# Kernel tuning notes

Hardware: AMD Instinct MI355X
Metric: run time of the kernel (lower is better)

Reference implementation:

```python
import jax, jax.numpy as jnp
import numpy as np

KNN_K = 8
WINDOW = 3  # temporal_window + 1 candidate frames
LN_EPS = 1e-5
NORM_EPS = 1e-12


def setup_inputs() -> dict:
    key = jax.random.key(0)
    B, T, M, D, H = 2, 8, 512, 1024, 1024
    ks = jax.random.split(key, 12)
    s = 0.02
    return {
        "z": jax.random.normal(ks[0], (B, T, M, D), jnp.float32),
        "Wq": jax.random.normal(ks[1], (D, D), jnp.float32) * s,
        "Wv": jax.random.normal(ks[2], (D, D), jnp.float32) * s,
        "Wout": jax.random.normal(ks[3], (D, D), jnp.float32) * s,
        "ln_w": jnp.ones((D,), jnp.float32),
        "ln_b": jnp.zeros((D,), jnp.float32),
        "Watt_q": jax.random.normal(ks[4], (D, D), jnp.float32) * s,
        "Watt_k": jax.random.normal(ks[5], (D, D), jnp.float32) * s,
        "W_ih": jax.random.normal(ks[6], (3 * H, D), jnp.float32) * s,
        "W_hh": jax.random.normal(ks[7], (3 * H, H), jnp.float32) * s,
        "b_ih": jnp.zeros((3 * H,), jnp.float32),
        "b_hh": jnp.zeros((3 * H,), jnp.float32),
        "W_mf": jax.random.normal(ks[8], (D, H), jnp.float32) * s,
        "b_mf": jnp.zeros((D,), jnp.float32),
    }


def _forward(z, Wq, Wv, Wout, ln_w, ln_b, Watt_q, Watt_k,
             W_ih, W_hh, b_ih, b_hh, W_mf, b_mf):
    B, T, M, D = z.shape
    H = W_hh.shape[1]
    # cosine normalization (torch F.normalize with eps clamp)
    zn = z / jnp.maximum(jnp.linalg.norm(z, axis=-1, keepdims=True), NORM_EPS)
    mem = jnp.zeros((B, M, H), z.dtype)
    b_ar = jnp.arange(B)[:, None, None]
    outs = []
    for t in range(T):  # T is static; fully vectorized over B, M, k inside
        tts = t - jnp.arange(WINDOW)          # candidate frames t, t-1, t-2
        valid = tts >= 0                      # [W]
        cand = zn[:, jnp.clip(tts, 0)]        # [B,W,M,D]
        # cosine similarity query nodes at t vs all candidates (dt-major order)
        sim = jnp.einsum('bmd,bwnd->bmwn', zn[:, t], cand).reshape(B, M, WINDOW * M)
        sim = jnp.where(jnp.repeat(valid, M)[None, None, :], sim, -jnp.inf)
        vals, idx = jax.lax.top_k(sim, KNN_K)  # [B,M,k]
        dt = idx // M
        j = idx % M
        tt = jnp.clip(t - dt, 0)
        Kfeat = z[b_ar, tt, j]                 # [B,M,k,D] gathered neighbors
        # GAT quirk faithful to source: scalar logit scale from node 0's query,
        # first output coordinate only, shared across all nodes of (b,t)
        s0 = z[:, t, 0] @ Watt_q[0]            # [B]
        kh_sum = (Kfeat @ Watt_k.T).sum(-1)    # [B,M,k]
        att = jax.nn.softmax(s0[:, None, None] * kh_sum, axis=-1)
        alpha = 0.5 * vals + 0.5 * att         # [B,M,k]
        msg = jnp.einsum('bmk,bmkd->bmd', alpha, Kfeat @ Wv.T)
        h_t = z[:, t]                          # [B,M,D]
        x = msg + h_t @ Wq.T
        mu = x.mean(-1, keepdims=True)
        var = ((x - mu) ** 2).mean(-1, keepdims=True)
        x = (x - mu) / jnp.sqrt(var + LN_EPS) * ln_w + ln_b
        inp = x @ Wout.T
        # torch GRUCell: gates ordered (r, z, n)
        gi = inp @ W_ih.T + b_ih               # [B,M,3H]
        gh = mem @ W_hh.T + b_hh
        ir, iz, inn = jnp.split(gi, 3, axis=-1)
        hr, hz, hn = jnp.split(gh, 3, axis=-1)
        r = jax.nn.sigmoid(ir + hr)
        zg = jax.nn.sigmoid(iz + hz)
        n = jnp.tanh(inn + r * hn)
        mem = (1.0 - zg) * n + zg * mem
        outs.append(h_t + mem @ W_mf.T + b_mf)
    h = jnp.stack(outs, axis=1)                # [B,T,M,D]
    return h, mem


def reference(z, Wq, Wv, Wout, ln_w, ln_b, Watt_q, Watt_k,
              W_ih, W_hh, b_ih, b_hh, W_mf, b_mf):
    return _forward(z, Wq, Wv, Wout, ln_w, ln_b, Watt_q, Watt_k,
                    W_ih, W_hh, b_ih, b_hh, W_mf, b_mf)
```

## Files before the change

### kernel.cpp

```cpp
#include <hip/hip_runtime.h>
#include <hip/hip_bf16.h>
#include <math.h>

#define B_ 2
#define T_ 8
#define M_ 512
#define D_ 1024
#define H_ 1024
#define NC_ 1536
#define KNN 8

typedef __hip_bfloat16 bf16;
typedef short v8s __attribute__((ext_vector_type(8)));
typedef float v4f __attribute__((ext_vector_type(4)));

__device__ __forceinline__ float b2f(short s) {
  union { unsigned u; float f; } x; x.u = ((unsigned)(unsigned short)s) << 16; return x.f;
}
__device__ __forceinline__ short f2b(float f) {
  bf16 h = __float2bfloat16(f); return *(short*)&h;
}

__device__ __forceinline__ void async16(const void* g, void* l) {
  __builtin_amdgcn_global_load_lds(
      (const __attribute__((address_space(1))) void*)g,
      (__attribute__((address_space(3))) void*)l, 16, 0, 0);
}

__device__ __forceinline__ void mfma_loop(const bf16* __restrict__ A,
                                          const bf16* __restrict__ Bp,
                                          int K, v4f (&acc)[4][4],
                                          bf16* sA, bf16* sB)
{
  const int tid  = threadIdx.x;
  const int lane = tid & 63;
  const int wave = tid >> 6;
  const int quad = lane >> 4;
  const int l15  = lane & 15;
  const int wr = (wave >> 1) * 64;
  const int wc = (wave & 1) * 64;

  const int r0 = tid >> 2, g0 = (tid & 3) ^ ((r0 >> 1) & 3);
  const int c1 = tid + 256;
  const int r1 = c1 >> 2,  g1 = (c1 & 3) ^ ((r1 >> 1) & 3);

  const bf16* a0p = A  + (size_t)r0*K + g0*8;
  const bf16* a1p = A  + (size_t)r1*K + g1*8;
  const bf16* b0p = Bp + (size_t)r0*K + g0*8;
  const bf16* b1p = Bp + (size_t)r1*K + g1*8;
  bf16* la0 = sA + tid*8;  bf16* la1 = sA + c1*8;
  bf16* lb0 = sB + tid*8;  bf16* lb1 = sB + c1*8;

  int aoff[4], boff[4];
  #pragma unroll
  for (int i = 0; i < 4; ++i) {
    int ra = wr + i*16 + l15;
    aoff[i] = (ra*4 + (quad ^ ((ra >> 1) & 3))) * 8;
    int rb = wc + i*16 + l15;
    boff[i] = (rb*4 + (quad ^ ((rb >> 1) & 3))) * 8;
  }

  for (int k0 = 0; k0 < K; k0 += 32) {
    __syncthreads();
    async16(a0p + k0, la0);
    async16(a1p + k0, la1);
    async16(b0p + k0, lb0);
    async16(b1p + k0, lb1);
    __syncthreads();
    v8s af[4], bfr[4];
    #pragma unroll
    for (int i = 0; i < 4; ++i) af[i]  = *(const v8s*)(sA + aoff[i]);
    #pragma unroll
    for (int i = 0; i < 4; ++i) bfr[i] = *(const v8s*)(sB + boff[i]);
    #pragma unroll
    for (int mi = 0; mi < 4; ++mi)
      #pragma unroll
      for (int ni = 0; ni < 4; ++ni)
        acc[mi][ni] = __builtin_amdgcn_mfma_f32_16x16x32_bf16(
            af[mi], bfr[ni], acc[mi][ni], 0, 0, 0);
  }
}

__device__ __forceinline__ void out_tile(int oid, int tp,
    const bf16* __restrict__ memhb, const bf16* __restrict__ Wmfb,
    const float* __restrict__ b_mf, const float* __restrict__ z,
    float* __restrict__ out, bf16* sA, bf16* sB)
{
  const int rb = oid >> 3, cb = oid & 7;
  const int g0 = (rb >> 2)*4096 + tp*512 + (rb & 3)*128;
  v4f acc[4][4];
  #pragma unroll
  for (int i = 0; i < 4; ++i)
    #pragma unroll
    for (int j = 0; j < 4; ++j) acc[i][j] = (v4f){0.f,0.f,0.f,0.f};
  mfma_loop(memhb + (size_t)g0*H_, Wmfb + (size_t)(cb*128)*H_, H_, acc, sA, sB);
  const int tid = threadIdx.x, lane = tid & 63, wave = tid >> 6;
  const int quad = lane >> 4, l15 = lane & 15;
  const int wr = (wave >> 1) * 64, wcc = (wave & 1) * 64;
  #pragma unroll
  for (int ni = 0; ni < 4; ++ni) {
    const int col = cb*128 + wcc + ni*16 + l15;
    const float bv = b_mf[col];
    #pragma unroll
    for (int mi = 0; mi < 4; ++mi) {
      const int rowb = g0 + wr + mi*16 + quad*4;
      #pragma unroll
      for (int reg = 0; reg < 4; ++reg) {
        const int row = rowb + reg;
        out[(size_t)row*D_ + col] = acc[mi][ni][reg] + bv + z[(size_t)row*D_ + col];
      }
    }
  }
}

template<bool DUAL, bool STATS>
__global__ __launch_bounds__(256) void k_bgemm(
    const bf16* __restrict__ A1, const bf16* __restrict__ B1,
    const bf16* __restrict__ A2, const bf16* __restrict__ B2,
    bf16* __restrict__ Cv, int N, int K,
    float* __restrict__ ssum, float* __restrict__ ssq)
{
  __shared__ bf16 sA[128*32];
  __shared__ bf16 sB[128*32];
  v4f acc[4][4];
  #pragma unroll
  for (int i = 0; i < 4; ++i)
    #pragma unroll
    for (int j = 0; j < 4; ++j) acc[i][j] = (v4f){0.f,0.f,0.f,0.f};

  const int row0 = blockIdx.y * 128, col0 = blockIdx.x * 128;
  mfma_loop(A1 + (size_t)row0*K, B1 + (size_t)col0*K, K, acc, sA, sB);
  if constexpr (DUAL)
    mfma_loop(A2 + (size_t)row0*K, B2 + (size_t)col0*K, K, acc, sA, sB);

  const int tid = threadIdx.x, lane = tid & 63, wave = tid >> 6;
  const int quad = lane >> 4, l15 = lane & 15;
  const int wr = (wave >> 1) * 64, wc = (wave & 1) * 64;

  float st_s[4][4], st_q[4][4];
  if constexpr (STATS) {
    #pragma unroll
    for (int a = 0; a < 4; ++a)
      #pragma unroll
      for (int b = 0; b < 4; ++b) { st_s[a][b] = 0.f; st_q[a][b] = 0.f; }
  }

  #pragma unroll
  for (int ni = 0; ni < 4; ++ni) {
    const int col = col0 + wc + ni*16 + l15;
    #pragma unroll
    for (int mi = 0; mi < 4; ++mi) {
      const int rowb = row0 + wr + mi*16 + quad*4;
      #pragma unroll
      for (int reg = 0; reg < 4; ++reg) {
        float v = acc[mi][ni][reg];
        if constexpr (STATS) { st_s[mi][reg] += v; st_q[mi][reg] += v*v; }
        Cv[(size_t)(rowb+reg)*N + col] = __float2bfloat16(v);
      }
    }
  }

  if constexpr (STATS) {
    const int p = blockIdx.x*2 + (wave & 1);
    #pragma unroll
    for (int mi = 0; mi < 4; ++mi)
      #pragma unroll
      for (int reg = 0; reg < 4; ++reg) {
        float s = st_s[mi][reg], q = st_q[mi][reg];
        #pragma unroll
        for (int o = 1; o < 16; o <<= 1) {
          s += __shfl_xor(s, o, 64);
          q += __shfl_xor(q, o, 64);
        }
        if (l15 == 0) {
          const int row = row0 + wr + mi*16 + quad*4 + reg;
          ssum[(size_t)p*8192 + row] = s;
          ssq [(size_t)p*8192 + row] = q;
        }
      }
  }
}

__global__ __launch_bounds__(256) void k_gic(
    const bf16* __restrict__ Xb, const bf16* __restrict__ Wcb,
    const float* __restrict__ ssum, const float* __restrict__ ssq,
    const float* __restrict__ u2, const float* __restrict__ v2b,
    bf16* __restrict__ Cv)
{
  __shared__ bf16 sA[128*32];
  __shared__ bf16 sB[128*32];
  __shared__ float smu[128], srs[128];
  const int row0 = blockIdx.y * 128, col0 = blockIdx.x * 128;
  const int tid = threadIdx.x;
  if (tid < 128) {
    int r = row0 + tid;
    float s = 0.f, q = 0.f;
    #pragma unroll
    for (int p = 0; p < 16; ++p) { s += ssum[(size_t)p*8192 + r]; q += ssq[(size_t)p*8192 + r]; }
    float mu = s * (1.f/D_);
    float var = q * (1.f/D_) - mu*mu;
    smu[tid] = mu; srs[tid] = rsqrtf(var + 1e-5f);
  }
  __syncthreads();

  v4f acc[4][4];
  #pragma unroll
  for (int i = 0; i < 4; ++i)
    #pragma unroll
    for (int j = 0; j < 4; ++j) acc[i][j] = (v4f){0.f,0.f,0.f,0.f};
  mfma_loop(Xb + (size_t)row0*D_, Wcb + (size_t)col0*D_, D_, acc, sA, sB);

  const int lane = tid & 63, wave = tid >> 6;
  const int quad = lane >> 4, l15 = lane & 15;
  const int wr = (wave >> 1) * 64, wc = (wave & 1) * 64;
  #pragma unroll
  for (int ni = 0; ni < 4; ++ni) {
    const int col = col0 + wc + ni*16 + l15;
    const float uj = u2[col], vj = v2b[col];
    #pragma unroll
    for (int mi = 0; mi < 4; ++mi) {
      const int rl = wr + mi*16 + quad*4;
      #pragma unroll
      for (int reg = 0; reg < 4; ++reg) {
        const float mu = smu[rl+reg], rs = srs[rl+reg];
        float v = rs*acc[mi][ni][reg] - mu*rs*uj + vj;
        Cv[(size_t)(row0+rl+reg)*(3*H_) + col] = __float2bfloat16(v);
      }
    }
  }
}

__global__ __launch_bounds__(256) void k_sims(const bf16* __restrict__ znhi,
                                              const bf16* __restrict__ znlo,
                                              const float* __restrict__ z,
                                              const float* __restrict__ wks,
                                              float* __restrict__ sim,
                                              float* __restrict__ kh,
                                              const bf16* __restrict__ Wihb,
                                              const float* __restrict__ Wout,
                                              const float* __restrict__ lnw,
                                              const float* __restrict__ u,
                                              const float* __restrict__ vv,
                                              const float* __restrict__ b_ih,
                                              bf16* __restrict__ Wcb,
                                              float* __restrict__ u2,
                                              float* __restrict__ v2b)
{
  __shared__ bf16 sAh[128*32];
  __shared__ bf16 sAl[128*32];
  __shared__ bf16 sBh[128*32];
  __shared__ bf16 sBl[128*32];

  const int zi = blockIdx.z;
  const int tid  = threadIdx.x;
  const int lane = tid & 63;
  const int wave = tid >> 6;

  if (zi >= 176) {
    const int slot = (zi - 176)*16 + blockIdx.y*4 + blockIdx.x;
    if (slot < 192) {
      const int yc = slot >> 3, xc = slot & 7;
      const int quad = lane >> 4, l15 = lane & 15;
      const int wr = (wave >> 1) * 64, wcc = (wave & 1) * 64;

      v4f acc[4][4];
      #pragma unroll
      for (int i = 0; i < 4; ++i)
        #pragma unroll
        for (int j = 0; j < 4; ++j) acc[i][j] = (v4f){0.f,0.f,0.f,0.f};

      const int r0 = tid >> 2, g0c = (tid & 3) ^ ((r0 >> 1) & 3);
      const int c1 = tid + 256, r1 = c1 >> 2, g1c = (c1 & 3) ^ ((r1 >> 1) & 3);
      const bf16* Ap = Wihb + (size_t)(yc*128)*D_;
      const size_t ao0 = (size_t)r0*D_ + g0c*8;
      const size_t ao1 = (size_t)r1*D_ + g1c*8;

      const int cB = tid >> 3;
      const int jg = (tid & 7) * 16;
      float lw[16];
      #pragma unroll
      for (int e = 0; e < 16; ++e) lw[e] = lnw[xc*128 + jg + e];

      int aoff[4], boff[4];
      #pragma unroll
      for (int i = 0; i < 4; ++i) {
        int ra = wr + i*16 + l15;
        aoff[i] = (ra*4 + (quad ^ ((ra >> 1) & 3))) * 8;
        int rb = wcc + i*16 + l15;
        boff[i] = (rb*4 + (quad ^ ((rb >> 1) & 3))) * 8;
      }

      for (int k0 = 0; k0 < D_; k0 += 32) {
        __syncthreads();
        async16(Ap + ao0 + k0, sAh + tid*8);
        async16(Ap + ao1 + k0, sAh + c1*8);
        const float* wsrc = Wout + (size_t)(k0 + cB)*D_ + xc*128 + jg;
        #pragma unroll
        for (int e4 = 0; e4 < 4; ++e4) {
          float4 wv = *(const float4*)(wsrc + e4*4);
          float vals[4] = {wv.x, wv.y, wv.z, wv.w};
          #pragma unroll
          for (int e = 0; e < 4; ++e) {
            int j = jg + e4*4 + e;
            int sl = (cB >> 3) ^ ((j >> 1) & 3);
            sBh[(j*4 + sl)*8 + (cB & 7)] = __float2bfloat16(vals[e]*lw[e4*4+e]);
          }
        }
        __syncthreads();
        v8s af[4], bfr[4];
        #pragma unroll
        for (int i = 0; i < 4; ++i) af[i]  = *(const v8s*)(sAh + aoff[i]);
        #pragma unroll
        for (int i = 0; i < 4; ++i) bfr[i] = *(const v8s*)(sBh + boff[i]);
        #pragma unroll
        for (int mi = 0; mi < 4; ++mi)
          #pragma unroll
          for (int ni = 0; ni < 4; ++ni)
            acc[mi][ni] = __builtin_amdgcn_mfma_f32_16x16x32_bf16(
                af[mi], bfr[ni], acc[mi][ni], 0, 0, 0);
      }
      #pragma unroll
      for (int ni = 0; ni < 4; ++ni) {
        const int col = xc*128 + wcc + ni*16 + l15;
        #pragma unroll
        for (int mi = 0; mi < 4; ++mi) {
          const int rowb = yc*128 + wr + mi*16 + quad*4;
          #pragma unroll
          for (int reg = 0; reg < 4; ++reg)
            Wcb[(size_t)(rowb+reg)*D_ + col] = __float2bfloat16(acc[mi][ni][reg]);
        }
      }
    } else {
      int g = (slot - 192)*256 + tid;
      if (g < 3*H_) {
        const bf16* wr_ = Wihb + (size_t)g*D_;
        float du = 0.f, dv = 0.f;
        for (int k = 0; k < 128; ++k) {
          v8s wv = *(const v8s*)(wr_ + k*8);
          #pragma unroll
          for (int e = 0; e < 8; ++e) {
            float wf = b2f(wv[e]);
            du += wf * u[k*8+e];
            dv += wf * vv[k*8+e];
          }
        }
        u2[g] = du; v2b[g] = dv + b_ih[g];
      }
    }
    return;
  }

  if (zi >= 48) {
    int kid = (zi - 48)*16 + blockIdx.y*4 + blockIdx.x;
    int r = kid*4 + wave;
    const float* zp = z + (size_t)r*D_ + lane*16;
    const float* wp = wks + lane*16;
    float p = 0.f;
    #pragma unroll
    for (int j = 0; j < 4; ++j) {
      float4 a = *(const float4*)(zp + j*4);
      float b4v[4] = {wp[j*4], wp[j*4+1], wp[j*4+2], wp[j*4+3]};
      p += a.x*b4v[0] + a.y*b4v[1] + a.z*b4v[2] + a.w*b4v[3];
    }
    for (int o = 32; o; o >>= 1) p += __shfl_down(p, o, 64);
    if (lane == 0) kh[r] = p;
    return;
  }

  const int w  = zi % 3;
  const int bt = zi / 3;
  const int b  = bt / T_;
  const int t  = bt % T_;
  if (w > t) return;
  const int tw = t - w;
  const int arow0 = bt*M_ + blockIdx.y*128;
  const int brow0 = (b*T_ + tw)*M_ + blockIdx.x*128;

  const bf16* Ah = znhi + (size_t)arow0*D_;
  const bf16* Al = znlo + (size_t)arow0*D_;
  const bf16* Bh = znhi + (size_t)brow0*D_;
  const bf16* Bl = znlo + (size_t)brow0*D_;

  v4f acc[4][4];
  #pragma unroll
  for (int i = 0; i < 4; ++i)
    #pragma unroll
    for (int j = 0; j < 4; ++j) acc[i][j] = (v4f){0.f,0.f,0.f,0.f};

  const int quad = lane >> 4;
  const int l15  = lane & 15;
  const int wr = (wave >> 1) * 64;
  const int wc = (wave & 1) * 64;

  const int r0 = tid >> 2, g0 = (tid & 3) ^ ((r0 >> 1) & 3);
  const int c1 = tid + 256;
  const int r1 = c1 >> 2,  g1 = (c1 & 3) ^ ((r1 >> 1) & 3);
  const size_t o0 = (size_t)r0*D_ + g0*8;
  const size_t o1 = (size_t)r1*D_ + g1*8;

  int aoff[4], boff[4];
  #pragma unroll
  for (int i = 0; i < 4; ++i) {
    int ra = wr + i*16 + l15;
    aoff[i] = (ra*4 + (quad ^ ((ra >> 1) & 3))) * 8;
    int rb = wc + i*16 + l15;
    boff[i] = (rb*4 + (quad ^ ((rb >> 1) & 3))) * 8;
  }

  for (int k0 = 0; k0 < D_; k0 += 32) {
    __syncthreads();
    async16(Ah + o0 + k0, sAh + tid*8);
    async16(Ah + o1 + k0, sAh + c1*8);
    async16(Al + o0 + k0, sAl + tid*8);
    async16(Al + o1 + k0, sAl + c1*8);
    async16(Bh + o0 + k0, sBh + tid*8);
    async16(Bh + o1 + k0, sBh + c1*8);
    async16(Bl + o0 + k0, sBl + tid*8);
    async16(Bl + o1 + k0, sBl + c1*8);
    __syncthreads();
    v8s ah[4], al[4], bh[4], bl[4];
    #pragma unroll
    for (int i = 0; i < 4; ++i) {
      ah[i] = *(const v8s*)(sAh + aoff[i]);
      al[i] = *(const v8s*)(sAl + aoff[i]);
      bh[i] = *(const v8s*)(sBh + boff[i]);
      bl[i] = *(const v8s*)(sBl + boff[i]);
    }
    #pragma unroll
    for (int mi = 0; mi < 4; ++mi)
      #pragma unroll
      for (int ni = 0; ni < 4; ++ni) {
        acc[mi][ni] = __builtin_amdgcn_mfma_f32_16x16x32_bf16(ah[mi], bh[ni], acc[mi][ni], 0, 0, 0);
        acc[mi][ni] = __builtin_amdgcn_mfma_f32_16x16x32_bf16(ah[mi], bl[ni], acc[mi][ni], 0, 0, 0);
        acc[mi][ni] = __builtin_amdgcn_mfma_f32_16x16x32_bf16(al[mi], bh[ni], acc[mi][ni], 0, 0, 0);
      }
  }

  float* C = sim + (size_t)bt*M_*NC_;
  const int rowbase = blockIdx.y*128 + wr;
  const int colbase = w*M_ + blockIdx.x*128 + wc;
  #pragma unroll
  for (int ni = 0; ni < 4; ++ni) {
    const int col = colbase + ni*16 + l15;
    #pragma unroll
    for (int mi = 0; mi < 4; ++mi) {
      const int rowb = rowbase + mi*16 + quad*4;
      #pragma unroll
      for (int reg = 0; reg < 4; ++reg)
        C[(size_t)(rowb+reg)*NC_ + col] = acc[mi][ni][reg];
    }
  }
}

__global__ __launch_bounds__(256) void k_fgru2(
    const bf16* __restrict__ membIn, const bf16* __restrict__ Whhb,
    const bf16* __restrict__ gib, const float* __restrict__ b_hh,
    float* __restrict__ mem, bf16* __restrict__ membOut,
    bf16* __restrict__ memhb, float* __restrict__ outT,
    const bf16* __restrict__ Wmfb, const float* __restrict__ b_mf,
    const float* __restrict__ z, float* __restrict__ outMain, int t)
{
  __shared__ bf16 smem[8192];

  if (blockIdx.y >= 16) {
    out_tile((blockIdx.y-16)*16 + blockIdx.x, t-1,
             memhb, Wmfb, b_mf, z, outMain, smem, smem + 4096);
    return;
  }

  bf16* sA = smem;
  const int row0 = blockIdx.y*64, col0 = blockIdx.x*64;

  const int tid  = threadIdx.x;
  const int lane = tid & 63;
  const int wave = tid >> 6;
  const int quad = lane >> 4;
  const int l15  = lane & 15;
  const int wr   = (wave >> 1) * 32;
  const int wcol = (wave & 1) * 32;

  const int rA = tid >> 2, gA = (tid & 3) ^ ((rA >> 1) & 3);
  const size_t aofs = (size_t)rA*H_ + gA*8;
  const size_t bofs = (size_t)(col0 + rA)*H_ + gA*8;

  int aoff[2], boff[2];
  #pragma unroll
  for (int i = 0; i < 2; ++i) {
    int ra = wr + i*16 + l15;
    aoff[i] = (ra*4 + (quad ^ ((ra >> 1) & 3))) * 8;
    int rb = wcol + i*16 + l15;
    boff[i] = (rb*4 + (quad ^ ((rb >> 1) & 3))) * 8;
  }

  v4f acc[3][2][2];
  #pragma unroll
  for (int g = 0; g < 3; ++g)
    #pragma unroll
    for (int i = 0; i < 2; ++i)
      #pragma unroll
      for (int j = 0; j < 2; ++j) acc[g][i][j] = (v4f){0.f,0.f,0.f,0.f};

  if (t > 0) {
    const bf16* prev = membIn + (size_t)row0*H_;
    for (int k0 = 0; k0 < H_; k0 += 32) {
      __syncthreads();
      async16(prev + aofs + k0, sA + tid*8);
      async16(Whhb + bofs + k0,           smem + 2048 + tid*8);
      async16(Whhb + 1048576 + bofs + k0, smem + 4096 + tid*8);
      async16(Whhb + 2097152 + bofs + k0, smem + 6144 + tid*8);
      __syncthreads();
      v8s af[2], bfr[3][2];
      #pragma unroll
      for (int i = 0; i < 2; ++i) af[i] = *(const v8s*)(sA + aoff[i]);
      #pragma unroll
      for (int g = 0; g < 3; ++g)
        #pragma unroll
        for (int i = 0; i < 2; ++i)
          bfr[g][i] = *(const v8s*)(smem + 2048 + g*2048 + boff[i]);
      #pragma unroll
      for (int g = 0; g < 3; ++g)
        #pragma unroll
        for (int mi = 0; mi < 2; ++mi)
          #pragma unroll
          for (int ni = 0; ni < 2; ++ni)
            acc[g][mi][ni] = __builtin_amdgcn_mfma_f32_16x16x32_bf16(
                af[mi], bfr[g][ni], acc[g][mi][ni], 0, 0, 0);
    }
  }

  #pragma unroll
  for (int ni = 0; ni < 2; ++ni) {
    const int col = col0 + wcol + ni*16 + l15;
    const float bhr = b_hh[col];
    const float bhz = b_hh[H_ + col];
    const float bhn = b_hh[2*H_ + col];
    #pragma unroll
    for (int mi = 0; mi < 2; ++mi) {
      const int rowb = row0 + wr + mi*16 + quad*4;
      #pragma unroll
      for (int reg = 0; reg < 4; ++reg) {
        const int row = rowb + reg;
        const int b = row >> 9, m = row & 511;
        const size_t btm = (size_t)((b*T_ + t)*M_ + m);
        const bf16* gp = gib + btm*(3*H_);
        float ir  = b2f(*(const short*)(gp + col));
        float iz  = b2f(*(const short*)(gp + H_ + col));
        float inn = b2f(*(const short*)(gp + 2*H_ + col));
        float hr = acc[0][mi][ni][reg] + bhr;
        float hz = acc[1][mi][ni][reg] + bhz;
        float hn = acc[2][mi][ni][reg] + bhn;
        float rgt = 1.f/(1.f + expf(-(ir + hr)));
        float zgt = 1.f/(1.f + expf(-(iz + hz)));
        float n   = tanhf(inn + rgt*hn);
        const size_t mo = (size_t)row*H_ + col;
        float mold = (t > 0) ? mem[mo] : 0.f;
        float mnew = (1.f - zgt)*n + zgt*mold;
        mem[mo] = mnew;
        bf16 mb = __float2bfloat16(mnew);
        membOut[mo] = mb;
        memhb[btm*H_ + col] = mb;
        if (t == T_-1) outT[mo] = mnew;
      }
    }
  }
}

__global__ __launch_bounds__(256) void k_outtail(
    const bf16* __restrict__ memhb, const bf16* __restrict__ Wmfb,
    const float* __restrict__ b_mf, const float* __restrict__ z,
    float* __restrict__ outMain)
{
  __shared__ bf16 smem[8192];
  out_tile(blockIdx.y*8 + blockIdx.x, T_-1, memhb, Wmfb, b_mf, z, outMain,
           smem, smem + 4096);
}

__global__ __launch_bounds__(256) void k_prep(
    const float* __restrict__ Wq, const float* __restrict__ Wv,
    const float* __restrict__ Wout, const float* __restrict__ Wih,
    const float* __restrict__ Whh, const float* __restrict__ Wmf,
    const float* __restrict__ lnw, const float* __restrict__ lnb,
    const float* __restrict__ Wattk, const float* __restrict__ Wattq,
    const float* __restrict__ z,
    bf16* __restrict__ Wdst, float* __restrict__ wks,
    float* __restrict__ u, float* __restrict__ vv, float* __restrict__ s0,
    bf16* __restrict__ zb, bf16* __restrict__ znhi, bf16* __restrict__ znlo)
{
  __shared__ float ps[4], pk[4];
  const int bid = blockIdx.x, tid = threadIdx.x;

  if (bid < 10240) {
    int i = bid*256 + tid;
    const float* src; int base;
    if      (i <  262144) { src = Wq;   base = 0; }
    else if (i <  524288) { src = Wv;   base = 262144; }
    else if (i <  786432) { src = Wout; base = 524288; }
    else if (i < 1572864) { src = Wih;  base = 786432; }
    else if (i < 2359296) { src = Whh;  base = 1572864; }
    else                  { src = Wmf;  base = 2359296; }
    float4 v = ((const float4*)src)[i - base];
    *(short4*)(Wdst + (size_t)i*4) = make_short4(f2b(v.x), f2b(v.y), f2b(v.z), f2b(v.w));
  } else if (bid < 10368) {
    int rc = bid - 10240;
    int rowc = rc >> 2, colc = rc & 3;
    int d = colc*256 + tid;
    float s = 0.f;
    for (int r = rowc*32; r < rowc*32 + 32; ++r) s += Wattk[(size_t)r*D_ + d];
    atomicAdd(&wks[d], s);
  } else if (bid < 10624) {
    int j = (bid - 10368)*4 + (tid >> 6);
    int l = tid & 63;
    const float* wr_ = Wout + (size_t)j*D_ + l*16;
    const float* aw = lnw + l*16;
    const float* ab = lnb + l*16;
    float pu = 0.f, pv = 0.f;
    #pragma unroll
    for (int q = 0; q < 4; ++q) {
      float4 a = *(const float4*)(wr_ + q*4);
      float4 x = *(const float4*)(aw + q*4);
      float4 y = *(const float4*)(ab + q*4);
      pu += a.x*x.x + a.y*x.y + a.z*x.z + a.w*x.w;
      pv += a.x*y.x + a.y*y.y + a.z*y.z + a.w*y.w;
    }
    for (int o = 32; o; o >>= 1) { pu += __shfl_down(pu, o, 64); pv += __shfl_down(pv, o, 64); }
    if (l == 0) { u[j] = pu; vv[j] = pv; }
  } else if (bid < 10640) {
    int bt = bid - 10624;
    int d = tid*4;
    float4 a = *(const float4*)(z + (size_t)bt*M_*D_ + d);
    float4 q = *(const float4*)(Wattq + d);
    float p = a.x*q.x + a.y*q.y + a.z*q.z + a.w*q.w;
    for (int o = 32; o; o >>= 1) p += __shfl_down(p, o, 64);
    if ((tid & 63) == 0) ps[tid >> 6] = p;
    __syncthreads();
    if (tid == 0) s0[bt] = ps[0]+ps[1]+ps[2]+ps[3];
  } else {
    int row = bid - 10640;
    const float* zr = z + (size_t)row*D_;
    int d = tid*4;
    float4 v = *(const float4*)(zr + d);
    float ss = v.x*v.x + v.y*v.y + v.z*v.z + v.w*v.w;
    for (int o = 32; o; o >>= 1) ss += __shfl_down(ss, o, 64);
    if ((tid & 63) == 0) pk[tid >> 6] = ss;
    __syncthreads();
    float s = pk[0]+pk[1]+pk[2]+pk[3];
    float rn = 1.0f / fmaxf(sqrtf(s), 1e-12f);
    *(short4*)(zb + (size_t)row*D_ + d) = make_short4(f2b(v.x), f2b(v.y), f2b(v.z), f2b(v.w));
    float zn[4] = {v.x*rn, v.y*rn, v.z*rn, v.w*rn};
    short hi[4], lo[4];
    #pragma unroll
    for (int j = 0; j < 4; ++j) {
      hi[j] = f2b(zn[j]);
      lo[j] = f2b(zn[j] - b2f(hi[j]));
    }
    *(short4*)(znhi + (size_t)row*D_ + d) = make_short4(hi[0],hi[1],hi[2],hi[3]);
    *(short4*)(znlo + (size_t)row*D_ + d) = make_short4(lo[0],lo[1],lo[2],lo[3]);
  }
}

__global__ __launch_bounds__(256) void k_topk(
    const float* __restrict__ sim, const float* __restrict__ kh,
    const float* __restrict__ s0, const bf16* __restrict__ zb,
    bf16* __restrict__ kbarb)
{
  const int wave = threadIdx.x >> 6, l = threadIdx.x & 63;
  const int r  = blockIdx.x*4 + wave;
  const int bt = r >> 9, m = r & 511;
  const int b  = bt >> 3, t = bt & 7;
  const float* srow = sim + (size_t)bt*M_*NC_ + (size_t)m*NC_;
  const int limit = (t >= 2) ? NC_ : ((t == 1) ? 2*M_ : M_);

  float v[24];
  #pragma unroll
  for (int j = 0; j < 24; ++j) {
    int i = j*64 + l;
    v[j] = (i < limit) ? srow[i] : -INFINITY;
  }

  float selv[KNN]; int seli[KNN];
  #pragma unroll
  for (int k = 0; k < KNN; ++k) {
    float bv = v[0]; int bj = 0;
    #pragma unroll
    for (int j = 1; j < 24; ++j)
      if (v[j] > bv) { bv = v[j]; bj = j; }
    int bi = bj*64 + l;
    #pragma unroll
    for (int o = 1; o < 64; o <<= 1) {
      float ov = __shfl_xor(bv, o, 64);
      int   oi = __shfl_xor(bi, o, 64);
      if (ov > bv || (ov == bv && oi < bi)) { bv = ov; bi = oi; }
    }
    selv[k] = bv; seli[k] = bi;
    if ((bi & 63) == l) {
      int jj = bi >> 6;
      #pragma unroll
      for (int j = 0; j < 24; ++j) if (j == jj) v[j] = -INFINITY;
    }
  }

  float khv = 0.f;
  if (l < KNN) {
    int idx = seli[l];
    int w = idx >> 9, n = idx & 511;
    int tt = t - w;
    khv = kh[(b*T_ + tt)*M_ + n];
  }
  float s0v = s0[bt];
  float att[KNN], mx = -INFINITY;
  #pragma unroll
  for (int k = 0; k < KNN; ++k) { att[k] = s0v * __shfl(khv, k, 64); mx = fmaxf(mx, att[k]); }
  float den = 0.f;
  #pragma unroll
  for (int k = 0; k < KNN; ++k) { att[k] = expf(att[k]-mx); den += att[k]; }
  float rden = 1.0f/den;
  float alpha[KNN];
  #pragma unroll
  for (int k = 0; k < KNN; ++k) alpha[k] = 0.5f*selv[k] + 0.5f*att[k]*rden;

  const int d0 = l*16;
  float o[16];
  #pragma unroll
  for (int e = 0; e < 16; ++e) o[e] = 0.f;
  #pragma unroll
  for (int k = 0; k < KNN; ++k) {
    int idx = seli[k];
    int w = idx >> 9, n = idx & 511;
    int tt = t - w;
    const bf16* zp = zb + ((size_t)((b*T_ + tt)*M_ + n))*D_ + d0;
    v8s z0 = *(const v8s*)zp;
    v8s z1 = *(const v8s*)(zp + 8);
    float al = alpha[k];
    #pragma unroll
    for (int e = 0; e < 8; ++e) {
      o[e]   = fmaf(al, b2f(z0[e]), o[e]);
      o[8+e] = fmaf(al, b2f(z1[e]), o[8+e]);
    }
  }
  bf16* kp = kbarb + (size_t)r*D_ + d0;
  short outv[16];
  #pragma unroll
  for (int e = 0; e < 16; ++e) outv[e] = f2b(o[e]);
  *(v8s*)kp       = *(v8s*)outv;
  *(v8s*)(kp + 8) = *(v8s*)(outv + 8);
}

extern "C" void kernel_launch(void* const* d_in, const int* in_sizes, int n_in,
                              void* d_out, int out_size, void* d_ws, size_t ws_size,
                              hipStream_t stream) {
  (void)in_sizes; (void)n_in; (void)out_size; (void)ws_size;
  const float* z      = (const float*)d_in[0];
  const float* Wq     = (const float*)d_in[1];
  const float* Wv     = (const float*)d_in[2];
  const float* Wout   = (const float*)d_in[3];
  const float* ln_w   = (const float*)d_in[4];
  const float* ln_b   = (const float*)d_in[5];
  const float* Watt_q = (const float*)d_in[6];
  const float* Watt_k = (const float*)d_in[7];
  const float* W_ih   = (const float*)d_in[8];
  const float* W_hh   = (const float*)d_in[9];
  const float* b_ih   = (const float*)d_in[10];
  const float* b_hh   = (const float*)d_in[11];
  const float* W_mf   = (const float*)d_in[12];
  const float* b_mf   = (const float*)d_in[13];
  float* out = (float*)d_out;
  float* ws  = (float*)d_ws;

  float* sim   = ws;
  bf16*  GIb   = (bf16*)ws;
  bf16*  znhi  = (bf16*)(ws + 12582912);
  bf16*  Xb    = znhi;
  bf16*  zb    = (bf16*)(ws + 16777216);
  bf16*  kbarb = (bf16*)(ws + 20971520);
  bf16*  memhb = (bf16*)(ws + 25165824);
  bf16*  znlo  = memhb;
  bf16*  mA    = (bf16*)(ws + 29360128);
  bf16*  mB    = (bf16*)(ws + 29884416);
  float* mem   = ws + 30408704;
  bf16*  Wqb   = (bf16*)(ws + 31457280);
  bf16*  Wvb   = Wqb + 1048576;
  bf16*  Wihb  = Wqb + 3145728;
  bf16*  Whhb  = Wqb + 6291456;
  bf16*  Wmfb  = Wqb + 9437184;
  float* wks   = ws + 36700160;
  float* s0    = ws + 36701184;
  float* kh    = ws + 36701200;
  float* u     = ws + 36709392;
  float* vv    = ws + 36710416;
  float* ssum  = ws + 36711440;
  float* ssq   = ws + 36842512;
  float* u2    = ws + 36973584;
  float* v2b   = ws + 36976656;
  bf16*  Wcb   = (bf16*)(ws + 36979728);

  hipMemsetAsync(wks, 0, 1024*sizeof(float), stream);

  k_prep<<<dim3(18832), dim3(256), 0, stream>>>(
      Wq, Wv, Wout, W_ih, W_hh, W_mf, ln_w, ln_b, Watt_k, Watt_q, z,
      Wqb, wks, u, vv, s0, zb, znhi, znlo);

  k_sims<<<dim3(4,4,189), dim3(256), 0, stream>>>(
      znhi, znlo, z, wks, sim, kh,
      Wihb, Wout, ln_w, u, vv, b_ih, Wcb, u2, v2b);

  k_topk<<<dim3(2048), dim3(256), 0, stream>>>(sim, kh, s0, zb, kbarb);

  k_bgemm<true,true><<<dim3(8,64), dim3(256), 0, stream>>>(
      kbarb, Wvb, zb, Wqb, Xb, D_, D_, ssum, ssq);

  k_gic<<<dim3(24,64), dim3(256), 0, stream>>>(Xb, Wcb, ssum, ssq, u2, v2b, GIb);

  for (int t = 0; t < T_; ++t) {
    bf16*       mout = (t & 1) ? mB : mA;
    const bf16* min_ = (t & 1) ? mA : mB;
    dim3 grid = (t == 0) ? dim3(16,16) : dim3(16,20);
    k_fgru2<<<grid, dim3(256), 0, stream>>>(
        min_, Whhb, GIb, b_hh, mem, mout, memhb,
        out + (size_t)B_*T_*M_*D_, Wmfb, b_mf, z, out, t);
  }

  k_outtail<<<dim3(8,8), dim3(256), 0, stream>>>(memhb, Wmfb, b_mf, z, out);
}
```

Baseline: 686.1 us.

## Exploit sim symmetry for same-frame tiles and pre-transpose Wout to bf16

The same-frame (w==0) cosine-similarity tiles are symmetric, so blocks below the diagonal now exit early and off-diagonal blocks also write their transposed tile, which skips about a third of the split-bf16 GEMM work for that window. Wout scaled by ln_w is transposed and converted to bf16 once in the prep kernel, so the fused Wih·Wout GEMM can use the shared async mfma_loop instead of converting fp32 on the fly. The mirrored writes are strided float4 stores that may coalesce poorly, and the prep kernel gains extra blocks and a large shared-memory transpose buffer.

```diff
diff --git a/kernel.cpp b/kernel.cpp
--- a/kernel.cpp
+++ b/kernel.cpp
@@ -237,8 +237,7 @@
                                               float* __restrict__ sim,
                                               float* __restrict__ kh,
                                               const bf16* __restrict__ Wihb,
-                                              const float* __restrict__ Wout,
-                                              const float* __restrict__ lnw,
+                                              const bf16* __restrict__ WoutTb,
                                               const float* __restrict__ u,
                                               const float* __restrict__ vv,
                                               const float* __restrict__ b_ih,
@@ -260,65 +259,15 @@
     const int slot = (zi - 176)*16 + blockIdx.y*4 + blockIdx.x;
     if (slot < 192) {
       const int yc = slot >> 3, xc = slot & 7;
-      const int quad = lane >> 4, l15 = lane & 15;
-      const int wr = (wave >> 1) * 64, wcc = (wave & 1) * 64;
-
       v4f acc[4][4];
       #pragma unroll
       for (int i = 0; i < 4; ++i)
         #pragma unroll
         for (int j = 0; j < 4; ++j) acc[i][j] = (v4f){0.f,0.f,0.f,0.f};
-
-      const int r0 = tid >> 2, g0c = (tid & 3) ^ ((r0 >> 1) & 3);
-      const int c1 = tid + 256, r1 = c1 >> 2, g1c = (c1 & 3) ^ ((r1 >> 1) & 3);
-      const bf16* Ap = Wihb + (size_t)(yc*128)*D_;
-      const size_t ao0 = (size_t)r0*D_ + g0c*8;
-      const size_t ao1 = (size_t)r1*D_ + g1c*8;
-
-      const int cB = tid >> 3;
-      const int jg = (tid & 7) * 16;
-      float lw[16];
-      #pragma unroll
-      for (int e = 0; e < 16; ++e) lw[e] = lnw[xc*128 + jg + e];
-
-      int aoff[4], boff[4];
-      #pragma unroll
-      for (int i = 0; i < 4; ++i) {
-        int ra = wr + i*16 + l15;
-        aoff[i] = (ra*4 + (quad ^ ((ra >> 1) & 3))) * 8;
-        int rb = wcc + i*16 + l15;
-        boff[i] = (rb*4 + (quad ^ ((rb >> 1) & 3))) * 8;
-      }
-
-      for (int k0 = 0; k0 < D_; k0 += 32) {
-        __syncthreads();
-        async16(Ap + ao0 + k0, sAh + tid*8);
-        async16(Ap + ao1 + k0, sAh + c1*8);
-        const float* wsrc = Wout + (size_t)(k0 + cB)*D_ + xc*128 + jg;
-        #pragma unroll
-        for (int e4 = 0; e4 < 4; ++e4) {
-          float4 wv = *(const float4*)(wsrc + e4*4);
-          float vals[4] = {wv.x, wv.y, wv.z, wv.w};
-          #pragma unroll
-          for (int e = 0; e < 4; ++e) {
-            int j = jg + e4*4 + e;
-            int sl = (cB >> 3) ^ ((j >> 1) & 3);
-            sBh[(j*4 + sl)*8 + (cB & 7)] = __float2bfloat16(vals[e]*lw[e4*4+e]);
-          }
-        }
-        __syncthreads();
-        v8s af[4], bfr[4];
-        #pragma unroll
-        for (int i = 0; i < 4; ++i) af[i]  = *(const v8s*)(sAh + aoff[i]);
-        #pragma unroll
-        for (int i = 0; i < 4; ++i) bfr[i] = *(const v8s*)(sBh + boff[i]);
-        #pragma unroll
-        for (int mi = 0; mi < 4; ++mi)
-          #pragma unroll
-          for (int ni = 0; ni < 4; ++ni)
-            acc[mi][ni] = __builtin_amdgcn_mfma_f32_16x16x32_bf16(
-                af[mi], bfr[ni], acc[mi][ni], 0, 0, 0);
-      }
+      mfma_loop(Wihb + (size_t)(yc*128)*D_, WoutTb + (size_t)(xc*128)*D_,
+                D_, acc, sAh, sBh);
+      const int quad = lane >> 4, l15 = lane & 15;
+      const int wr = (wave >> 1) * 64, wcc = (wave & 1) * 64;
       #pragma unroll
       for (int ni = 0; ni < 4; ++ni) {
         const int col = xc*128 + wcc + ni*16 + l15;
@@ -359,8 +308,8 @@
     #pragma unroll
     for (int j = 0; j < 4; ++j) {
       float4 a = *(const float4*)(zp + j*4);
-      float b4v[4] = {wp[j*4], wp[j*4+1], wp[j*4+2], wp[j*4+3]};
-      p += a.x*b4v[0] + a.y*b4v[1] + a.z*b4v[2] + a.w*b4v[3];
+      float4 b = *(const float4*)(wp + j*4);
+      p += a.x*b.x + a.y*b.y + a.z*b.z + a.w*b.w;
     }
     for (int o = 32; o; o >>= 1) p += __shfl_down(p, o, 64);
     if (lane == 0) kh[r] = p;
@@ -372,6 +321,7 @@
   const int b  = bt / T_;
   const int t  = bt % T_;
   if (w > t) return;
+  if (w == 0 && blockIdx.y > blockIdx.x) return;
   const int tw = t - w;
   const int arow0 = bt*M_ + blockIdx.y*128;
   const int brow0 = (b*T_ + tw)*M_ + blockIdx.x*128;
@@ -439,6 +389,7 @@
   float* C = sim + (size_t)bt*M_*NC_;
   const int rowbase = blockIdx.y*128 + wr;
   const int colbase = w*M_ + blockIdx.x*128 + wc;
+  const bool mir = (w == 0) && (blockIdx.y != blockIdx.x);
   #pragma unroll
   for (int ni = 0; ni < 4; ++ni) {
     const int col = colbase + ni*16 + l15;
@@ -448,6 +399,8 @@
       #pragma unroll
       for (int reg = 0; reg < 4; ++reg)
         C[(size_t)(rowb+reg)*NC_ + col] = acc[mi][ni][reg];
+      if (mir)
+        *(float4*)(C + (size_t)col*NC_ + rowb) = *(float4*)&acc[mi][ni];
     }
   }
 }
@@ -584,9 +537,11 @@
     const float* __restrict__ z,
     bf16* __restrict__ Wdst, float* __restrict__ wks,
     float* __restrict__ u, float* __restrict__ vv, float* __restrict__ s0,
-    bf16* __restrict__ zb, bf16* __restrict__ znhi, bf16* __restrict__ znlo)
+    bf16* __restrict__ zb, bf16* __restrict__ znhi, bf16* __restrict__ znlo,
+    bf16* __restrict__ WoutTb)
 {
   __shared__ float ps[4], pk[4];
+  __shared__ bf16 tr[128*130];
   const int bid = blockIdx.x, tid = threadIdx.x;
 
   if (bid < 10240) {
@@ -634,7 +589,7 @@
     if ((tid & 63) == 0) ps[tid >> 6] = p;
     __syncthreads();
     if (tid == 0) s0[bt] = ps[0]+ps[1]+ps[2]+ps[3];
-  } else {
+  } else if (bid < 18832) {
     int row = bid - 10640;
     const float* zr = z + (size_t)row*D_;
     int d = tid*4;
@@ -655,6 +610,32 @@
     }
     *(short4*)(znhi + (size_t)row*D_ + d) = make_short4(hi[0],hi[1],hi[2],hi[3]);
     *(short4*)(znlo + (size_t)row*D_ + d) = make_short4(lo[0],lo[1],lo[2],lo[3]);
+  } else {
+    int idx = bid - 18832;
+    int bi = idx >> 3, bd = idx & 7;
+    int c4 = tid & 31, rr = tid >> 5;
+    float4 lw4 = *(const float4*)(lnw + bd*128 + c4*4);
+    #pragma unroll 4
+    for (int it = 0; it < 16; ++it) {
+      int i = it*8 + rr;
+      float4 v = *(const float4*)(Wout + (size_t)(bi*128+i)*D_ + bd*128 + c4*4);
+      int d0 = c4*4;
+      tr[(d0+0)*130 + i] = __float2bfloat16(v.x*lw4.x);
+      tr[(d0+1)*130 + i] = __float2bfloat16(v.y*lw4.y);
+      tr[(d0+2)*130 + i] = __float2bfloat16(v.z*lw4.z);
+      tr[(d0+3)*130 + i] = __float2bfloat16(v.w*lw4.w);
+    }
+    __syncthreads();
+    #pragma unroll 4
+    for (int it = 0; it < 16; ++it) {
+      int d = it*8 + rr;
+      short4 o;
+      o.x = *(short*)&tr[d*130 + c4*4+0];
+      o.y = *(short*)&tr[d*130 + c4*4+1];
+      o.z = *(short*)&tr[d*130 + c4*4+2];
+      o.w = *(short*)&tr[d*130 + c4*4+3];
+      *(short4*)(WoutTb + (size_t)(bd*128+d)*D_ + bi*128 + c4*4) = o;
+    }
   }
 }
 
@@ -792,16 +773,17 @@
   float* u2    = ws + 36973584;
   float* v2b   = ws + 36976656;
   bf16*  Wcb   = (bf16*)(ws + 36979728);
+  bf16*  WoutTb= (bf16*)(ws + 38552592);
 
   hipMemsetAsync(wks, 0, 1024*sizeof(float), stream);
 
-  k_prep<<<dim3(18832), dim3(256), 0, stream>>>(
+  k_prep<<<dim3(18896), dim3(256), 0, stream>>>(
       Wq, Wv, Wout, W_ih, W_hh, W_mf, ln_w, ln_b, Watt_k, Watt_q, z,
-      Wqb, wks, u, vv, s0, zb, znhi, znlo);
+      Wqb, wks, u, vv, s0, zb, znhi, znlo, WoutTb);
 
   k_sims<<<dim3(4,4,189), dim3(256), 0, stream>>>(
       znhi, znlo, z, wks, sim, kh,
-      Wihb, Wout, ln_w, u, vv, b_ih, Wcb, u2, v2b);
+      Wihb, WoutTb, u, vv, b_ih, Wcb, u2, v2b);
 
   k_topk<<<dim3(2048), dim3(256), 0, stream>>>(sim, kh, s0, zb, kbarb);
 
```

Result: no change. 679.4 us (-1.0%).
